# Performance work log

Hardware: AMD Instinct MI355X
Metric: run time of the kernel (lower is better)

Reference implementation:

```python
import jax, jax.numpy as jnp
import numpy as np

PAD_IDX = 0

def _gru_layer(xs, W_ih, W_hh, b_ih, b_hh):
    # xs: [B, S, D]; W_ih: [3H, D]; W_hh: [3H, H]
    B = xs.shape[0]
    H = W_hh.shape[1]
    # precompute input-side gate projections for all timesteps: [S, B, 3H]
    xg = jnp.einsum('bsd,gd->sbg', xs, W_ih) + b_ih

    def step(h, xg_t):
        hg = h @ W_hh.T + b_hh                      # [B, 3H]
        xr, xz, xn = jnp.split(xg_t, 3, axis=-1)
        hr, hz, hn = jnp.split(hg, 3, axis=-1)
        r = jax.nn.sigmoid(xr + hr)
        z = jax.nn.sigmoid(xz + hz)
        n = jnp.tanh(xn + r * hn)
        h_new = (1.0 - z) * n + z * h
        return h_new, h_new

    h0 = jnp.zeros((B, H), dtype=xs.dtype)
    _, ys = jax.lax.scan(step, h0, xg)              # ys: [S, B, H]
    return jnp.transpose(ys, (1, 0, 2))             # [B, S, H]

def setup_inputs() -> dict:
    key = jax.random.key(0)
    ks = jax.random.split(key, 12)
    V, E, H = 32000, 256, 512
    B, S = 64, 512
    s_e = 1.0 / np.sqrt(H)
    inp = {
        'x': jax.random.randint(ks[0], (B, S), 0, V, dtype=jnp.int32),
        'emb': jax.random.normal(ks[1], (V, E), dtype=jnp.float32),
        'W_ih0': jax.random.uniform(ks[2], (3 * H, E), jnp.float32, -s_e, s_e),
        'W_hh0': jax.random.uniform(ks[3], (3 * H, H), jnp.float32, -s_e, s_e),
        'b_ih0': jax.random.uniform(ks[4], (3 * H,), jnp.float32, -s_e, s_e),
        'b_hh0': jax.random.uniform(ks[5], (3 * H,), jnp.float32, -s_e, s_e),
        'W_ih1': jax.random.uniform(ks[6], (3 * H, H), jnp.float32, -s_e, s_e),
        'W_hh1': jax.random.uniform(ks[7], (3 * H, H), jnp.float32, -s_e, s_e),
        'b_ih1': jax.random.uniform(ks[8], (3 * H,), jnp.float32, -s_e, s_e),
        'b_hh1': jax.random.uniform(ks[9], (3 * H,), jnp.float32, -s_e, s_e),
        'W_fc': jax.random.uniform(ks[10], (1, H), jnp.float32, -s_e, s_e),
        'b_fc': jax.random.uniform(ks[11], (1,), jnp.float32, -s_e, s_e),
    }
    return inp

def reference(x, emb, W_ih0, W_hh0, b_ih0, b_hh0, W_ih1, W_hh1, b_ih1, b_hh1, W_fc, b_fc):
    # embedding with padding_idx: pad row is zero
    emb_z = emb.at[PAD_IDX].set(0.0)
    h = emb_z[x]                                    # [B, S, E]
    h = _gru_layer(h, W_ih0, W_hh0, b_ih0, b_hh0)   # [B, S, H]
    h = _gru_layer(h, W_ih1, W_hh1, b_ih1, b_hh1)   # [B, S, H]
    final = h[:, -1, :]                             # [B, H]
    return jax.nn.sigmoid(final @ W_fc.T + b_fc)    # [B, 1]
```

## Files before the change

### kernel.cpp

```cpp
#include <hip/hip_runtime.h>
#include <math.h>

typedef short  s8v __attribute__((ext_vector_type(8)));
typedef float  f4v __attribute__((ext_vector_type(4)));
typedef unsigned long long ull;

#define S_LEN 512
#define BATCH 64
#define HID   512
#define TPB   256

#define WI0H_OFF 0L
#define WI0L_OFF 786432L
#define WH0H_OFF 1572864L
#define WH0L_OFF 3145728L
#define WI1H_OFF 4718592L
#define WI1L_OFF 6291456L
#define WH1H_OFF 7864320L
#define WH1L_OFF 9437184L
#define XEB_OFF  11010048L
#define H0R_OFF  27787264L
#define H1R_OFF  94896128L
#define NEED_FAST 95420416L

#define BAR_BYTES   4096
#define HBUF_BYTES  (HID*BATCH*4)
#define A_OFF       BAR_BYTES
#define B_OFF       (A_OFF + 2*HBUF_BYTES)
#define XE_OFF      (B_OFF + 2*HBUF_BYTES)
#define XE_BYTES    ((size_t)S_LEN*64*BATCH*16)

__device__ __forceinline__ float fexp2(float x){ return __builtin_amdgcn_exp2f(x); }
__device__ __forceinline__ float frcp (float x){ return __builtin_amdgcn_rcpf(x); }
__device__ __forceinline__ float sigm (float x){ return frcp(1.f + fexp2(-1.44269504089f*x)); }
__device__ __forceinline__ float tanhx(float x){ return 1.f - 2.f*frcp(1.f + fexp2(2.88539008178f*x)); }
__device__ __forceinline__ float sigmoid_f(float v){ return 1.0f/(1.0f + expf(-v)); }

__device__ __forceinline__ unsigned short f2bf(float f){
  unsigned int u = __float_as_uint(f);
  u = u + 0x7FFFu + ((u >> 16) & 1u);
  return (unsigned short)(u >> 16);
}
__device__ __forceinline__ float bf2f(unsigned short s){
  return __uint_as_float(((unsigned int)s) << 16);
}

__global__ void wcvt_kernel(const float* __restrict__ Wih0, const float* __restrict__ Whh0,
                            const float* __restrict__ Wih1, const float* __restrict__ Whh1,
                            char* __restrict__ ws)
{
  int idx = blockIdx.x * TPB + threadIdx.x;
  const float* src; long hi_off, lo_off; int pos;
  if (idx < 393216)       { src = Wih0; pos = idx;           hi_off = WI0H_OFF; lo_off = WI0L_OFF; }
  else if (idx < 1179648) { src = Whh0; pos = idx - 393216;  hi_off = WH0H_OFF; lo_off = WH0L_OFF; }
  else if (idx < 1966080) { src = Wih1; pos = idx - 1179648; hi_off = WI1H_OFF; lo_off = WI1L_OFF; }
  else                    { src = Whh1; pos = idx - 1966080; hi_off = WH1H_OFF; lo_off = WH1L_OFF; }
  float w = src[pos];
  unsigned short h = f2bf(w);
  unsigned short l = f2bf(w - bf2f(h));
  ((unsigned short*)(ws + hi_off))[pos] = h;
  ((unsigned short*)(ws + lo_off))[pos] = l;
}

__global__ void gather_xe_bf_kernel(const int* __restrict__ x,
                                    const float* __restrict__ emb,
                                    char* __restrict__ ws)
{
  int idx = blockIdx.x * TPB + threadIdx.x;
  int k4 = idx & 63;
  int n  = idx >> 6;
  int t = n >> 6, b = n & 63;
  int tok = x[b * S_LEN + t];
  float4 v = make_float4(0.f,0.f,0.f,0.f);
  if (tok != 0) v = ((const float4*)emb)[(size_t)tok * 64 + k4];
  unsigned int lo = (unsigned int)f2bf(v.x) | ((unsigned int)f2bf(v.y) << 16);
  unsigned int hi = (unsigned int)f2bf(v.z) | ((unsigned int)f2bf(v.w) << 16);
  ((uint2*)(ws + XEB_OFF))[(long)n * 64 + k4] = make_uint2(lo, hi);
}

__device__ __forceinline__ void st_rec(ull* p, ull v){
  __hip_atomic_store(p, v, __ATOMIC_RELAXED, __HIP_MEMORY_SCOPE_AGENT);
}

template<int NKS>
__device__ __forceinline__ void load_ct(const ull* __restrict__ sl, int b,
                                        int quad, int k0s, unsigned want,
                                        s8v* __restrict__ bf)
{
  ull d[NKS][4];
  for (;;){
    #pragma unroll
    for (int ks = 0; ks < NKS; ++ks){
      const int e = k0s + ks*4 + quad;
      const ull* p = sl + (long)(4*e)*64 + b;
      #pragma unroll
      for (int i = 0; i < 4; ++i)
        d[ks][i] = __hip_atomic_load(p + (long)i*64, __ATOMIC_RELAXED, __HIP_MEMORY_SCOPE_AGENT);
    }
    bool ok = true;
    #pragma unroll
    for (int ks = 0; ks < NKS; ++ks)
      #pragma unroll
      for (int i = 0; i < 4; ++i)
        ok = ok && ((unsigned)(d[ks][i] >> 32) == want);
    if (__all(ok)) break;
    __builtin_amdgcn_s_sleep(1);
  }
  #pragma unroll
  for (int ks = 0; ks < NKS; ++ks){
    s8v v;
    #pragma unroll
    for (int i = 0; i < 4; ++i){
      unsigned lo = (unsigned)d[ks][i];
      v[2*i]   = (short)(lo & 0xFFFFu);
      v[2*i+1] = (short)(lo >> 16);
    }
    bf[ks] = v;
  }
}

template<int NKS, int ROLE>
__device__ __forceinline__ void scan_body(
    int isL1, int rowWG, int bh, int wave, int lane, int tid, int j0, int b0,
    const s8v* __restrict__ Whi, const s8v* __restrict__ Wlo, int AKs, int k0s,
    const s8v* __restrict__ xsrc,
    const ull* __restrict__ rsrc, int slotMask,
    const float* __restrict__ bih, const float* __restrict__ bhh,
    ull* __restrict__ rout, int outMask,
    f4v* __restrict__ part)
{
  const int quad = lane >> 4, col = lane & 15;

  s8v ahi[3][NKS], alo[3][NKS];
  #pragma unroll
  for (int rt = 0; rt < 3; ++rt){
    const int row = rt*512 + j0 + col;
    #pragma unroll
    for (int ks = 0; ks < NKS; ++ks){
      const int e = row*AKs + k0s + ks*4 + quad;
      ahi[rt][ks] = Whi[e];
      alo[rt][ks] = Wlo[e];
    }
  }

  float cr[4], cz[4], cnx[4], cnh[4], hp[4];
  #pragma unroll
  for (int r4 = 0; r4 < 4; ++r4){
    int j = j0 + wave*4 + r4;
    cr[r4]  = bih[j]      + bhh[j];
    cz[r4]  = bih[512+j]  + bhh[512+j];
    cnx[r4] = bih[1024+j];
    cnh[r4] = bhh[1024+j];
    hp[r4]  = 0.f;
  }

  for (int t = 0; t < S_LEN; ++t){
    f4v acc[3][2];
    #pragma unroll
    for (int rt = 0; rt < 3; ++rt){ acc[rt][0] = (f4v)0.f; acc[rt][1] = (f4v)0.f; }

    const bool active = (ROLE != 1) || (t > 0);
    if (active){
      const ull* sl = (ROLE == 1) ? rsrc + (long)((t-1) & slotMask)*16384
                                  : rsrc + (long)(t & slotMask)*16384;
      const unsigned want = (ROLE == 1) ? (unsigned)t : (unsigned)(t+1);
      #pragma unroll
      for (int ct = 0; ct < 2; ++ct){
        s8v bf[NKS];
        if (ROLE == 0){
          const int nG = b0 + ct*16 + col;
          const long base = ((long)t*64 + nG)*32 + k0s + quad;
          #pragma unroll
          for (int ks = 0; ks < NKS; ++ks) bf[ks] = xsrc[base + ks*4];
        } else {
          load_ct<NKS>(sl, b0 + ct*16 + col, quad, k0s, want, bf);
        }
        #pragma unroll
        for (int ks = 0; ks < NKS; ++ks)
          #pragma unroll
          for (int rt = 0; rt < 3; ++rt){
            acc[rt][ct] = __builtin_amdgcn_mfma_f32_16x16x32_bf16(ahi[rt][ks], bf[ks], acc[rt][ct], 0, 0, 0);
            acc[rt][ct] = __builtin_amdgcn_mfma_f32_16x16x32_bf16(alo[rt][ks], bf[ks], acc[rt][ct], 0, 0, 0);
          }
      }
    }

    #pragma unroll
    for (int rt = 0; rt < 3; ++rt)
      #pragma unroll
      for (int ct = 0; ct < 2; ++ct)
        part[(wave*6 + rt*2 + ct)*64 + lane] = acc[rt][ct];
    __syncthreads();

    if (lane < 32){
      const int b = lane;
      const int pl = wave*16 + (b & 15);
      const int ct = b >> 4;
      f4v sr = (f4v)0.f, sz = (f4v)0.f, snx = (f4v)0.f, snh = (f4v)0.f;
      #pragma unroll
      for (int w = 0; w < 4; ++w){
        const bool inpW = isL1 ? (w < 2) : (w >= 2);
        f4v g0 = part[(w*6 + 0*2 + ct)*64 + pl];
        f4v g1 = part[(w*6 + 1*2 + ct)*64 + pl];
        f4v g2 = part[(w*6 + 2*2 + ct)*64 + pl];
        sr += g0; sz += g1;
        if (inpW) snx += g2; else snh += g2;
      }
      unsigned short hb[4];
      #pragma unroll
      for (int r4 = 0; r4 < 4; ++r4){
        float r = sigm(sr[r4] + cr[r4]);
        float z = sigm(sz[r4] + cz[r4]);
        float n = tanhx(snx[r4] + cnx[r4] + r*(snh[r4] + cnh[r4]));
        float h = n + z*(hp[r4] - n);
        hp[r4] = h;
        hb[r4] = f2bf(h);
      }
      const int slotw = t & outMask;
      const ull tg = ((ull)(unsigned)(t + 1)) << 32;
      ull* ob = rout + (long)slotw*16384 + (long)(rowWG*8 + wave*2)*64 + (b0 + b);
      st_rec(ob,      ((ull)((unsigned)hb[0] | ((unsigned)hb[1] << 16))) | tg);
      st_rec(ob + 64, ((ull)((unsigned)hb[2] | ((unsigned)hb[3] << 16))) | tg);
    }
    __syncthreads();
  }
}

__global__ __launch_bounds__(TPB, 1) void gru_mfma_kernel(
    const float* __restrict__ bih0, const float* __restrict__ bhh0,
    const float* __restrict__ bih1, const float* __restrict__ bhh1,
    const float* __restrict__ Wfc,  const float* __restrict__ bfc,
    float* __restrict__ out, char* __restrict__ ws)
{
  __shared__ f4v part[4*6*64];

  const int tid  = threadIdx.x;
  const int wg   = blockIdx.x;
  const int lane = tid & 63;
  const int wave = tid >> 6;
  const int isL1 = (wg >= 64);
  const int lw   = wg & 63;
  const int rowWG = lw >> 1;
  const int bh    = lw & 1;
  const int j0 = rowWG * 16;
  const int b0 = bh * 32;

  const s8v* wi0h = (const s8v*)(ws + WI0H_OFF); const s8v* wi0l = (const s8v*)(ws + WI0L_OFF);
  const s8v* wh0h = (const s8v*)(ws + WH0H_OFF); const s8v* wh0l = (const s8v*)(ws + WH0L_OFF);
  const s8v* wi1h = (const s8v*)(ws + WI1H_OFF); const s8v* wi1l = (const s8v*)(ws + WI1L_OFF);
  const s8v* wh1h = (const s8v*)(ws + WH1H_OFF); const s8v* wh1l = (const s8v*)(ws + WH1L_OFF);
  const s8v* xeb = (const s8v*)(ws + XEB_OFF);
  const ull* h0r = (const ull*)(ws + H0R_OFF);
  const ull* h1r = (const ull*)(ws + H1R_OFF);
  ull* h0w = (ull*)(ws + H0R_OFF);
  ull* h1w = (ull*)(ws + H1R_OFF);

  if (!isL1){
    if (wave < 2)
      scan_body<8,1>(isL1, rowWG, bh, wave, lane, tid, j0, b0,
                     wh0h, wh0l, 64, wave*32, xeb, h0r, 0x3FFFFFFF,
                     bih0, bhh0, h0w, 0x3FFFFFFF, part);
    else
      scan_body<4,0>(isL1, rowWG, bh, wave, lane, tid, j0, b0,
                     wi0h, wi0l, 32, (wave-2)*16, xeb, h0r, 0x3FFFFFFF,
                     bih0, bhh0, h0w, 0x3FFFFFFF, part);
  } else {
    if (wave < 2)
      scan_body<8,2>(isL1, rowWG, bh, wave, lane, tid, j0, b0,
                     wi1h, wi1l, 64, wave*32, xeb, h0r, 0x3FFFFFFF,
                     bih1, bhh1, h1w, 3, part);
    else
      scan_body<8,1>(isL1, rowWG, bh, wave, lane, tid, j0, b0,
                     wh1h, wh1l, 64, (wave-2)*32, xeb, h1r, 3,
                     bih1, bhh1, h1w, 3, part);
  }

  if (wg == 64 && wave == 0){
    const ull* sl = h1r + 3L*16384;
    float acc = bfc[0];
    for (int c0 = 0; c0 < 256; c0 += 32){
      ull d[32];
      for (;;){
        #pragma unroll
        for (int i = 0; i < 32; ++i)
          d[i] = __hip_atomic_load(sl + (long)(c0+i)*64 + lane,
                                   __ATOMIC_RELAXED, __HIP_MEMORY_SCOPE_AGENT);
        bool ok = true;
        #pragma unroll
        for (int i = 0; i < 32; ++i) ok = ok && ((unsigned)(d[i] >> 32) == 512u);
        if (__all(ok)) break;
        __builtin_amdgcn_s_sleep(1);
      }
      #pragma unroll
      for (int i = 0; i < 32; ++i){
        unsigned lo = (unsigned)d[i];
        int u = (c0 + i) * 2;
        acc += bf2f((unsigned short)(lo & 0xFFFFu)) * Wfc[u]
             + bf2f((unsigned short)(lo >> 16))     * Wfc[u+1];
      }
    }
    out[lane] = sigm(acc);
  }
}

__global__ void gather_xe_kernel(const int* __restrict__ x,
                                 const float* __restrict__ emb,
                                 float4* __restrict__ xe4)
{
  int idx = blockIdx.x * TPB + threadIdx.x;
  int b  = idx & 63;
  int k4 = (idx >> 6) & 63;
  int t  = idx >> 12;
  int tok = x[b * S_LEN + t];
  float4 v = make_float4(0.f, 0.f, 0.f, 0.f);
  if (tok != 0) v = ((const float4*)emb)[(size_t)tok * 64 + k4];
  xe4[idx] = v;
}

__device__ __forceinline__ void accum_vec(const float4* __restrict__ xin,
                                          const float4* __restrict__ w0,
                                          const float4* __restrict__ w1,
                                          const float4* __restrict__ w2,
                                          int n4, int lane,
                                          float& ar, float& az, float& an)
{
  #pragma unroll 4
  for (int k = 0; k < n4; ++k){
    float4 xv = xin[k * 64 + lane];
    float4 wr = w0[k], wz = w1[k], wn = w2[k];
    ar = fmaf(xv.x, wr.x, ar); az = fmaf(xv.x, wz.x, az); an = fmaf(xv.x, wn.x, an);
    ar = fmaf(xv.y, wr.y, ar); az = fmaf(xv.y, wz.y, az); an = fmaf(xv.y, wn.y, an);
    ar = fmaf(xv.z, wr.z, ar); az = fmaf(xv.z, wz.z, az); an = fmaf(xv.z, wn.z, an);
    ar = fmaf(xv.w, wr.w, ar); az = fmaf(xv.w, wz.w, az); an = fmaf(xv.w, wn.w, an);
  }
}

__device__ __forceinline__ void accum_emb(const int* __restrict__ x,
                                          const float* __restrict__ emb, int t,
                                          const float4* __restrict__ w0,
                                          const float4* __restrict__ w1,
                                          const float4* __restrict__ w2,
                                          int lane, float& ar, float& az, float& an)
{
  int tok = x[lane * S_LEN + t];
  const float4* erow = (const float4*)emb + (size_t)tok * 64;
  float m = (tok != 0) ? 1.0f : 0.0f;
  #pragma unroll 4
  for (int k = 0; k < 64; ++k){
    float4 xv = erow[k];
    float xx = xv.x*m, xy = xv.y*m, xz = xv.z*m, xw = xv.w*m;
    float4 wr = w0[k], wz = w1[k], wn = w2[k];
    ar = fmaf(xx, wr.x, ar); az = fmaf(xx, wz.x, az); an = fmaf(xx, wn.x, an);
    ar = fmaf(xy, wr.y, ar); az = fmaf(xy, wz.y, az); an = fmaf(xy, wn.y, an);
    ar = fmaf(xz, wr.z, ar); az = fmaf(xz, wz.z, az); an = fmaf(xz, wn.z, an);
    ar = fmaf(xw, wr.w, ar); az = fmaf(xw, wz.w, az); an = fmaf(xw, wn.w, an);
  }
}

__device__ __forceinline__ void stage_weights(float4* wlds, int tid, int j0, int kin4,
                                              const float* Wih, const float* Whh)
{
  const int per = 3 * (kin4 + 128);
  for (int idx = tid; idx < 4 * per; idx += TPB){
    int w = idx / per, rem = idx - w * per;
    int g = rem / (kin4 + 128), k = rem - g * (kin4 + 128);
    int row = g * HID + j0 + w;
    float4 v;
    if (k < kin4) v = ((const float4*)Wih)[(size_t)row * kin4 + k];
    else          v = ((const float4*)Whh)[(size_t)row * 128 + (k - kin4)];
    wlds[(w * 3 + g) * 256 + k] = v;
  }
}

__device__ __forceinline__ void barrier_tick(int* bar, int wg, int tid, int phase)
{
  __syncthreads();
  if (tid == 0){
    __builtin_amdgcn_fence(__ATOMIC_RELEASE, "agent");
    int* leaf = bar + 32 + (wg >> 4) * 32;
    int old = __hip_atomic_fetch_add(leaf, 1, __ATOMIC_ACQ_REL, __HIP_MEMORY_SCOPE_AGENT);
    if (old == phase * 16 + 15){
      __hip_atomic_fetch_add(bar, 1, __ATOMIC_ACQ_REL, __HIP_MEMORY_SCOPE_AGENT);
    }
    const int target = (phase + 1) * 16;
    while (__hip_atomic_load(bar, __ATOMIC_ACQUIRE, __HIP_MEMORY_SCOPE_AGENT) < target){
      __builtin_amdgcn_s_sleep(2);
    }
    __builtin_amdgcn_fence(__ATOMIC_ACQUIRE, "agent");
  }
  __syncthreads();
}

__device__ __forceinline__ void finish_store(const float4* __restrict__ hprev,
                                             float ar, float az, float anx, float anh,
                                             int lane, int j, float4* __restrict__ hout)
{
  float r  = sigmoid_f(ar);
  float zz = sigmoid_f(az);
  float n  = tanhf(fmaf(r, anh, anx));
  int fi = ((j >> 2) * 64 + lane) * 4 + (j & 3);
  float hhp = ((const float*)hprev)[fi];
  ((float*)hout)[fi] = fmaf(zz, hhp - n, n);
}

__global__ __launch_bounds__(TPB) void gru_persist_kernel(
    const int*   __restrict__ x,    const float* __restrict__ emb,
    const float* __restrict__ Wih0, const float* __restrict__ Whh0,
    const float* __restrict__ bih0, const float* __restrict__ bhh0,
    const float* __restrict__ Wih1, const float* __restrict__ Whh1,
    const float* __restrict__ bih1, const float* __restrict__ bhh1,
    const float* __restrict__ Wfc,  const float* __restrict__ bfc,
    float* __restrict__ out, int* __restrict__ bar,
    float4* __restrict__ A0, float4* __restrict__ A1,
    float4* __restrict__ B0, float4* __restrict__ B1,
    const float4* __restrict__ xe4, int use_xe)
{
  __shared__ float4 wlds[3072];
  const int tid  = threadIdx.x;
  const int wg   = blockIdx.x;
  const int lane = tid & 63;
  const int wave = tid >> 6;
  const bool isL1 = (wg >= 128);
  const int j0   = (isL1 ? wg - 128 : wg) * 4;
  const int kin4 = isL1 ? 128 : 64;

  stage_weights(wlds, tid, j0, kin4, isL1 ? Wih1 : Wih0, isL1 ? Whh1 : Whh0);
  __syncthreads();

  const int j = j0 + wave;
  const float* bih = isL1 ? bih1 : bih0;
  const float* bhh = isL1 ? bhh1 : bhh0;
  const float br  = bih[j]        + bhh[j];
  const float bz  = bih[j + 512]  + bhh[j + 512];
  const float bnx = bih[j + 1024];
  const float bnh = bhh[j + 1024];

  const float4* w0 = &wlds[(wave * 3 + 0) * 256];
  const float4* w1 = &wlds[(wave * 3 + 1) * 256];
  const float4* w2 = &wlds[(wave * 3 + 2) * 256];

  float4* A[2] = {A0, A1};
  float4* B[2] = {B0, B1};

  for (int t = 0; t <= S_LEN; ++t){
    if (!isL1){
      if (t < S_LEN){
        const float4* hprev = A[(t + 1) & 1];
        float ar = br, az = bz, anx = bnx, anh = bnh;
        if (use_xe) accum_vec(xe4 + (size_t)t * 4096, w0, w1, w2, 64, lane, ar, az, anx);
        else        accum_emb(x, emb, t, w0, w1, w2, lane, ar, az, anx);
        accum_vec(hprev, w0 + 64, w1 + 64, w2 + 64, 128, lane, ar, az, anh);
        finish_store(hprev, ar, az, anx, anh, lane, j, A[t & 1]);
      }
    } else if (t >= 1){
      const int u = t - 1;
      const float4* xin   = A[u & 1];
      const float4* hprev = B[(u + 1) & 1];
      float ar = br, az = bz, anx = bnx, anh = bnh;
      accum_vec(xin,   w0,       w1,       w2,       128, lane, ar, az, anx);
      accum_vec(hprev, w0 + 128, w1 + 128, w2 + 128, 128, lane, ar, az, anh);
      finish_store(hprev, ar, az, anx, anh, lane, j, B[u & 1]);
    }
    barrier_tick(bar, wg, tid, t);
  }

  if (wg == 0 && wave == 0){
    float acc = bfc[0];
    const float4* h1 = B[1];
    const float4* wf = (const float4*)Wfc;
    #pragma unroll 4
    for (int k = 0; k < 128; ++k){
      float4 hv = h1[k * 64 + lane];
      float4 wv = wf[k];
      acc = fmaf(hv.x, wv.x, acc); acc = fmaf(hv.y, wv.y, acc);
      acc = fmaf(hv.z, wv.z, acc); acc = fmaf(hv.w, wv.w, acc);
    }
    out[lane] = sigmoid_f(acc);
  }
}

extern "C" void kernel_launch(void* const* d_in, const int* in_sizes, int n_in,
                              void* d_out, int out_size, void* d_ws, size_t ws_size,
                              hipStream_t stream)
{
  (void)in_sizes; (void)n_in; (void)out_size;
  const int*   x    = (const int*)  d_in[0];
  const float* emb  = (const float*)d_in[1];
  const float* Wih0 = (const float*)d_in[2];
  const float* Whh0 = (const float*)d_in[3];
  const float* bih0 = (const float*)d_in[4];
  const float* bhh0 = (const float*)d_in[5];
  const float* Wih1 = (const float*)d_in[6];
  const float* Whh1 = (const float*)d_in[7];
  const float* bih1 = (const float*)d_in[8];
  const float* bhh1 = (const float*)d_in[9];
  const float* Wfc  = (const float*)d_in[10];
  const float* bfc  = (const float*)d_in[11];
  float* out = (float*)d_out;
  char* ws = (char*)d_ws;

  if (ws_size >= (size_t)NEED_FAST){
    wcvt_kernel<<<2752512 / TPB, TPB, 0, stream>>>(Wih0, Whh0, Wih1, Whh1, ws);
    gather_xe_bf_kernel<<<2097152 / TPB, TPB, 0, stream>>>(x, emb, ws);
    gru_mfma_kernel<<<128, TPB, 0, stream>>>(bih0, bhh0, bih1, bhh1, Wfc, bfc, out, ws);
  } else {
    int*    bar = (int*)ws;
    float4* A0  = (float4*)(ws + A_OFF);
    float4* A1  = (float4*)(ws + A_OFF + HBUF_BYTES);
    float4* B0  = (float4*)(ws + B_OFF);
    float4* B1  = (float4*)(ws + B_OFF + HBUF_BYTES);
    float4* xe4 = (float4*)(ws + XE_OFF);
    const int use_xe = (ws_size >= (size_t)XE_OFF + XE_BYTES) ? 1 : 0;
    hipMemsetAsync(ws, 0, XE_OFF, stream);
    if (use_xe){
      gather_xe_kernel<<<(S_LEN * 64 * BATCH) / TPB, TPB, 0, stream>>>(x, emb, xe4);
    }
    gru_persist_kernel<<<256, TPB, 0, stream>>>(
        x, emb, Wih0, Whh0, bih0, bhh0, Wih1, Whh1, bih1, bhh1, Wfc, bfc,
        out, bar, A0, A1, B0, B1, xe4, use_xe);
  }
}
```

Before: 2.036 ms.

## Transpose recurrent state layout, vectorize tagged loads/stores, double-buffer LDS partials

```diff
diff --git a/kernel.cpp b/kernel.cpp
--- a/kernel.cpp
+++ b/kernel.cpp
@@ -3,6 +3,7 @@
 
 typedef short  s8v __attribute__((ext_vector_type(8)));
 typedef float  f4v __attribute__((ext_vector_type(4)));
+typedef unsigned int u4v __attribute__((ext_vector_type(4)));
 typedef unsigned long long ull;
 
 #define S_LEN 512
@@ -78,47 +79,6 @@
   ((uint2*)(ws + XEB_OFF))[(long)n * 64 + k4] = make_uint2(lo, hi);
 }
 
-__device__ __forceinline__ void st_rec(ull* p, ull v){
-  __hip_atomic_store(p, v, __ATOMIC_RELAXED, __HIP_MEMORY_SCOPE_AGENT);
-}
-
-template<int NKS>
-__device__ __forceinline__ void load_ct(const ull* __restrict__ sl, int b,
-                                        int quad, int k0s, unsigned want,
-                                        s8v* __restrict__ bf)
-{
-  ull d[NKS][4];
-  for (;;){
-    #pragma unroll
-    for (int ks = 0; ks < NKS; ++ks){
-      const int e = k0s + ks*4 + quad;
-      const ull* p = sl + (long)(4*e)*64 + b;
-      #pragma unroll
-      for (int i = 0; i < 4; ++i)
-        d[ks][i] = __hip_atomic_load(p + (long)i*64, __ATOMIC_RELAXED, __HIP_MEMORY_SCOPE_AGENT);
-    }
-    bool ok = true;
-    #pragma unroll
-    for (int ks = 0; ks < NKS; ++ks)
-      #pragma unroll
-      for (int i = 0; i < 4; ++i)
-        ok = ok && ((unsigned)(d[ks][i] >> 32) == want);
-    if (__all(ok)) break;
-    __builtin_amdgcn_s_sleep(1);
-  }
-  #pragma unroll
-  for (int ks = 0; ks < NKS; ++ks){
-    s8v v;
-    #pragma unroll
-    for (int i = 0; i < 4; ++i){
-      unsigned lo = (unsigned)d[ks][i];
-      v[2*i]   = (short)(lo & 0xFFFFu);
-      v[2*i+1] = (short)(lo >> 16);
-    }
-    bf[ks] = v;
-  }
-}
-
 template<int NKS, int ROLE>
 __device__ __forceinline__ void scan_body(
     int isL1, int rowWG, int bh, int wave, int lane, int tid, int j0, int b0,
@@ -159,21 +119,69 @@
     #pragma unroll
     for (int rt = 0; rt < 3; ++rt){ acc[rt][0] = (f4v)0.f; acc[rt][1] = (f4v)0.f; }
 
-    const bool active = (ROLE != 1) || (t > 0);
-    if (active){
-      const ull* sl = (ROLE == 1) ? rsrc + (long)((t-1) & slotMask)*16384
-                                  : rsrc + (long)(t & slotMask)*16384;
-      const unsigned want = (ROLE == 1) ? (unsigned)t : (unsigned)(t+1);
+    if (ROLE == 0){
       #pragma unroll
       for (int ct = 0; ct < 2; ++ct){
+        const int nG = b0 + ct*16 + col;
+        const long base = ((long)t*64 + nG)*32 + k0s + quad;
         s8v bf[NKS];
-        if (ROLE == 0){
-          const int nG = b0 + ct*16 + col;
-          const long base = ((long)t*64 + nG)*32 + k0s + quad;
+        #pragma unroll
+        for (int ks = 0; ks < NKS; ++ks) bf[ks] = xsrc[base + ks*4];
+        #pragma unroll
+        for (int ks = 0; ks < NKS; ++ks)
           #pragma unroll
-          for (int ks = 0; ks < NKS; ++ks) bf[ks] = xsrc[base + ks*4];
-        } else {
-          load_ct<NKS>(sl, b0 + ct*16 + col, quad, k0s, want, bf);
+          for (int rt = 0; rt < 3; ++rt){
+            acc[rt][ct] = __builtin_amdgcn_mfma_f32_16x16x32_bf16(ahi[rt][ks], bf[ks], acc[rt][ct], 0, 0, 0);
+            acc[rt][ct] = __builtin_amdgcn_mfma_f32_16x16x32_bf16(alo[rt][ks], bf[ks], acc[rt][ct], 0, 0, 0);
+          }
+      }
+    } else if ((ROLE != 1) || (t > 0)){
+      const int slot = (ROLE == 1) ? ((t-1) & slotMask) : (t & slotMask);
+      const unsigned want = (ROLE == 1) ? (unsigned)t : (unsigned)(t+1);
+      const ull* sl = rsrc + (long)slot*16384;
+
+      {
+        const ull* pp = sl + (long)(b0 + (lane & 31))*256 + (4*k0s + 2*lane);
+        for (;;){
+          u4v pv;
+          asm volatile("global_load_dwordx4 %0, %1, off sc0 sc1\n\t"
+                       "s_waitcnt vmcnt(0)"
+                       : "=&v"(pv) : "v"(pp) : "memory");
+          if (__all((pv.y == want) && (pv.w == want))) break;
+          __builtin_amdgcn_s_sleep(2);
+        }
+      }
+
+      #pragma unroll
+      for (int ct = 0; ct < 2; ++ct){
+        const int b = b0 + ct*16 + col;
+        const ull* bb = sl + (long)b*256 + (4*k0s + 4*quad);
+        s8v bf[NKS];
+        for (;;){
+          u4v q0[NKS], q1[NKS];
+          #pragma unroll
+          for (int ks = 0; ks < NKS; ++ks){
+            const ull* a = bb + 16*ks;
+            asm volatile("global_load_dwordx4 %0, %1, off sc0 sc1"
+                         : "=&v"(q0[ks]) : "v"(a) : "memory");
+            asm volatile("global_load_dwordx4 %0, %1, off sc0 sc1"
+                         : "=&v"(q1[ks]) : "v"(a + 2) : "memory");
+          }
+          asm volatile("s_waitcnt vmcnt(0)" ::: "memory");
+          bool ok = true;
+          #pragma unroll
+          for (int ks = 0; ks < NKS; ++ks)
+            ok = ok && (q0[ks].y == want) && (q0[ks].w == want)
+                    && (q1[ks].y == want) && (q1[ks].w == want);
+          if (__all(ok)){
+            #pragma unroll
+            for (int ks = 0; ks < NKS; ++ks){
+              u4v tv; tv.x = q0[ks].x; tv.y = q0[ks].z; tv.z = q1[ks].x; tv.w = q1[ks].z;
+              bf[ks] = *(s8v*)&tv;
+            }
+            break;
+          }
+          __builtin_amdgcn_s_sleep(2);
         }
         #pragma unroll
         for (int ks = 0; ks < NKS; ++ks)
@@ -185,11 +193,12 @@
       }
     }
 
+    const int pb = t & 1;
     #pragma unroll
     for (int rt = 0; rt < 3; ++rt)
       #pragma unroll
       for (int ct = 0; ct < 2; ++ct)
-        part[(wave*6 + rt*2 + ct)*64 + lane] = acc[rt][ct];
+        part[((pb*4 + wave)*6 + rt*2 + ct)*64 + lane] = acc[rt][ct];
     __syncthreads();
 
     if (lane < 32){
@@ -200,9 +209,9 @@
       #pragma unroll
       for (int w = 0; w < 4; ++w){
         const bool inpW = isL1 ? (w < 2) : (w >= 2);
-        f4v g0 = part[(w*6 + 0*2 + ct)*64 + pl];
-        f4v g1 = part[(w*6 + 1*2 + ct)*64 + pl];
-        f4v g2 = part[(w*6 + 2*2 + ct)*64 + pl];
+        f4v g0 = part[((pb*4 + w)*6 + 0*2 + ct)*64 + pl];
+        f4v g1 = part[((pb*4 + w)*6 + 1*2 + ct)*64 + pl];
+        f4v g2 = part[((pb*4 + w)*6 + 2*2 + ct)*64 + pl];
         sr += g0; sz += g1;
         if (inpW) snx += g2; else snh += g2;
       }
@@ -217,12 +226,13 @@
         hb[r4] = f2bf(h);
       }
       const int slotw = t & outMask;
-      const ull tg = ((ull)(unsigned)(t + 1)) << 32;
-      ull* ob = rout + (long)slotw*16384 + (long)(rowWG*8 + wave*2)*64 + (b0 + b);
-      st_rec(ob,      ((ull)((unsigned)hb[0] | ((unsigned)hb[1] << 16))) | tg);
-      st_rec(ob + 64, ((ull)((unsigned)hb[2] | ((unsigned)hb[3] << 16))) | tg);
-    }
-    __syncthreads();
+      const unsigned tg = (unsigned)(t + 1);
+      u4v sv;
+      sv.x = (unsigned)hb[0] | ((unsigned)hb[1] << 16); sv.y = tg;
+      sv.z = (unsigned)hb[2] | ((unsigned)hb[3] << 16); sv.w = tg;
+      ull* ob = rout + (long)slotw*16384 + (long)(b0 + b)*256 + (rowWG*8 + wave*2);
+      asm volatile("global_store_dwordx4 %0, %1, off sc0 sc1" :: "v"(ob), "v"(sv) : "memory");
+    }
   }
 }
 
@@ -232,7 +242,7 @@
     const float* __restrict__ Wfc,  const float* __restrict__ bfc,
     float* __restrict__ out, char* __restrict__ ws)
 {
-  __shared__ f4v part[4*6*64];
+  __shared__ f4v part[3072];
 
   const int tid  = threadIdx.x;
   const int wg   = blockIdx.x;
@@ -276,15 +286,14 @@
   }
 
   if (wg == 64 && wave == 0){
-    const ull* sl = h1r + 3L*16384;
+    const ull* bb = h1r + 3L*16384 + (long)lane*256;
     float acc = bfc[0];
     for (int c0 = 0; c0 < 256; c0 += 32){
       ull d[32];
       for (;;){
         #pragma unroll
         for (int i = 0; i < 32; ++i)
-          d[i] = __hip_atomic_load(sl + (long)(c0+i)*64 + lane,
-                                   __ATOMIC_RELAXED, __HIP_MEMORY_SCOPE_AGENT);
+          d[i] = __hip_atomic_load(bb + c0 + i, __ATOMIC_RELAXED, __HIP_MEMORY_SCOPE_AGENT);
         bool ok = true;
         #pragma unroll
         for (int i = 0; i < 32; ++i) ok = ok && ((unsigned)(d[i] >> 32) == 512u);
```

Measured after the change: 3.238 ms. 1.59x slower.

## Add per-group progress flags and double-buffer partials to drop second block barrier

Applied to the files above, without the earlier changes.

```diff
diff --git a/kernel.cpp b/kernel.cpp
--- a/kernel.cpp
+++ b/kernel.cpp
@@ -21,7 +21,8 @@
 #define XEB_OFF  11010048L
 #define H0R_OFF  27787264L
 #define H1R_OFF  94896128L
-#define NEED_FAST 95420416L
+#define FLG_OFF  95420416L
+#define NEED_FAST 95422464L
 
 #define BAR_BYTES   4096
 #define HBUF_BYTES  (HID*BATCH*4)
@@ -81,31 +82,36 @@
 __device__ __forceinline__ void st_rec(ull* p, ull v){
   __hip_atomic_store(p, v, __ATOMIC_RELAXED, __HIP_MEMORY_SCOPE_AGENT);
 }
+__device__ __forceinline__ void hint_wait(const unsigned* fl, int lane, unsigned target){
+  const unsigned* p = fl + (lane & 31);
+  for (;;){
+    unsigned v = __hip_atomic_load(p, __ATOMIC_RELAXED, __HIP_MEMORY_SCOPE_AGENT);
+    if (__all(v >= target)) break;
+    __builtin_amdgcn_s_sleep(1);
+  }
+}
 
 template<int NKS>
-__device__ __forceinline__ void load_ct(const ull* __restrict__ sl, int b,
-                                        int quad, int k0s, unsigned want,
-                                        s8v* __restrict__ bf)
+__device__ __forceinline__ bool try_load(const ull* __restrict__ sl, int b,
+                                         int quad, int k0s, unsigned want,
+                                         s8v* __restrict__ bf)
 {
   ull d[NKS][4];
-  for (;;){
+  #pragma unroll
+  for (int ks = 0; ks < NKS; ++ks){
+    const int e = k0s + ks*4 + quad;
+    const ull* p = sl + (long)(4*e)*64 + b;
     #pragma unroll
-    for (int ks = 0; ks < NKS; ++ks){
-      const int e = k0s + ks*4 + quad;
-      const ull* p = sl + (long)(4*e)*64 + b;
-      #pragma unroll
-      for (int i = 0; i < 4; ++i)
-        d[ks][i] = __hip_atomic_load(p + (long)i*64, __ATOMIC_RELAXED, __HIP_MEMORY_SCOPE_AGENT);
-    }
-    bool ok = true;
+    for (int i = 0; i < 4; ++i)
+      d[ks][i] = __hip_atomic_load(p + (long)i*64, __ATOMIC_RELAXED, __HIP_MEMORY_SCOPE_AGENT);
+  }
+  bool ok = true;
+  #pragma unroll
+  for (int ks = 0; ks < NKS; ++ks)
     #pragma unroll
-    for (int ks = 0; ks < NKS; ++ks)
-      #pragma unroll
-      for (int i = 0; i < 4; ++i)
-        ok = ok && ((unsigned)(d[ks][i] >> 32) == want);
-    if (__all(ok)) break;
-    __builtin_amdgcn_s_sleep(1);
-  }
+    for (int i = 0; i < 4; ++i)
+      ok = ok && ((unsigned)(d[ks][i] >> 32) == want);
+  if (!__all(ok)) return false;
   #pragma unroll
   for (int ks = 0; ks < NKS; ++ks){
     s8v v;
@@ -117,17 +123,18 @@
     }
     bf[ks] = v;
   }
+  return true;
 }
 
 template<int NKS, int ROLE>
 __device__ __forceinline__ void scan_body(
-    int isL1, int rowWG, int bh, int wave, int lane, int tid, int j0, int b0,
+    int isL1, int rowWG, int bh, int wave, int lane, int j0, int b0,
     const s8v* __restrict__ Whi, const s8v* __restrict__ Wlo, int AKs, int k0s,
     const s8v* __restrict__ xsrc,
     const ull* __restrict__ rsrc, int slotMask,
     const float* __restrict__ bih, const float* __restrict__ bhh,
     ull* __restrict__ rout, int outMask,
-    f4v* __restrict__ part)
+    char* __restrict__ ws, f4v* __restrict__ part, unsigned* __restrict__ cnt)
 {
   const int quad = lane >> 4, col = lane & 15;
 
@@ -154,26 +161,50 @@
     hp[r4]  = 0.f;
   }
 
+  const int pollLayer = (ROLE == 2) ? 0 : isL1;
+  const unsigned* flg = (const unsigned*)(ws + FLG_OFF)
+                        + ((pollLayer*2 + bh)*4 + (rowWG & 3))*32;
+  unsigned* fpub = (unsigned*)(ws + FLG_OFF) + ((isL1*2 + bh)*4)*32 + rowWG;
+
   for (int t = 0; t < S_LEN; ++t){
     f4v acc[3][2];
     #pragma unroll
     for (int rt = 0; rt < 3; ++rt){ acc[rt][0] = (f4v)0.f; acc[rt][1] = (f4v)0.f; }
 
-    const bool active = (ROLE != 1) || (t > 0);
-    if (active){
-      const ull* sl = (ROLE == 1) ? rsrc + (long)((t-1) & slotMask)*16384
-                                  : rsrc + (long)(t & slotMask)*16384;
-      const unsigned want = (ROLE == 1) ? (unsigned)t : (unsigned)(t+1);
+    if (ROLE == 0){
       #pragma unroll
       for (int ct = 0; ct < 2; ++ct){
+        const int nG = b0 + ct*16 + col;
+        const long base = ((long)t*64 + nG)*32 + k0s + quad;
         s8v bf[NKS];
-        if (ROLE == 0){
-          const int nG = b0 + ct*16 + col;
-          const long base = ((long)t*64 + nG)*32 + k0s + quad;
+        #pragma unroll
+        for (int ks = 0; ks < NKS; ++ks) bf[ks] = xsrc[base + ks*4];
+        #pragma unroll
+        for (int ks = 0; ks < NKS; ++ks)
           #pragma unroll
-          for (int ks = 0; ks < NKS; ++ks) bf[ks] = xsrc[base + ks*4];
+          for (int rt = 0; rt < 3; ++rt){
+            acc[rt][ct] = __builtin_amdgcn_mfma_f32_16x16x32_bf16(ahi[rt][ks], bf[ks], acc[rt][ct], 0, 0, 0);
+            acc[rt][ct] = __builtin_amdgcn_mfma_f32_16x16x32_bf16(alo[rt][ks], bf[ks], acc[rt][ct], 0, 0, 0);
+          }
+      }
+    } else if ((ROLE != 1) || (t > 0)){
+      const int slot = (ROLE == 1) ? ((t-1) & slotMask) : (t & slotMask);
+      const unsigned want = (ROLE == 1) ? (unsigned)t : (unsigned)(t+1);
+      const ull* sl = rsrc + (long)slot*16384;
+      #pragma unroll
+      for (int ct = 0; ct < 2; ++ct){
+        const int b = b0 + ct*16 + col;
+        s8v bf[NKS];
+        if (ROLE == 2){
+          if (!try_load<NKS>(sl, b, quad, k0s, want, bf)){
+            hint_wait(flg, lane, want);
+            while (!try_load<NKS>(sl, b, quad, k0s, want, bf))
+              __builtin_amdgcn_s_sleep(1);
+          }
         } else {
-          load_ct<NKS>(sl, b0 + ct*16 + col, quad, k0s, want, bf);
+          if (ct == 0) hint_wait(flg, lane, want);
+          while (!try_load<NKS>(sl, b, quad, k0s, want, bf))
+            __builtin_amdgcn_s_sleep(1);
         }
         #pragma unroll
         for (int ks = 0; ks < NKS; ++ks)
@@ -185,11 +216,12 @@
       }
     }
 
+    const int pb = t & 1;
     #pragma unroll
     for (int rt = 0; rt < 3; ++rt)
       #pragma unroll
       for (int ct = 0; ct < 2; ++ct)
-        part[(wave*6 + rt*2 + ct)*64 + lane] = acc[rt][ct];
+        part[((pb*4 + wave)*6 + rt*2 + ct)*64 + lane] = acc[rt][ct];
     __syncthreads();
 
     if (lane < 32){
@@ -200,9 +232,9 @@
       #pragma unroll
       for (int w = 0; w < 4; ++w){
         const bool inpW = isL1 ? (w < 2) : (w >= 2);
-        f4v g0 = part[(w*6 + 0*2 + ct)*64 + pl];
-        f4v g1 = part[(w*6 + 1*2 + ct)*64 + pl];
-        f4v g2 = part[(w*6 + 2*2 + ct)*64 + pl];
+        f4v g0 = part[((pb*4 + w)*6 + 0*2 + ct)*64 + pl];
+        f4v g1 = part[((pb*4 + w)*6 + 1*2 + ct)*64 + pl];
+        f4v g2 = part[((pb*4 + w)*6 + 2*2 + ct)*64 + pl];
         sr += g0; sz += g1;
         if (inpW) snx += g2; else snh += g2;
       }
@@ -222,7 +254,15 @@
       st_rec(ob,      ((ull)((unsigned)hb[0] | ((unsigned)hb[1] << 16))) | tg);
       st_rec(ob + 64, ((ull)((unsigned)hb[2] | ((unsigned)hb[3] << 16))) | tg);
     }
-    __syncthreads();
+    if (lane == 0){
+      unsigned old = atomicAdd(cnt, 1u);
+      if (old == 4u*(unsigned)t + 3u){
+        #pragma unroll
+        for (int rp = 0; rp < 4; ++rp)
+          __hip_atomic_store(fpub + rp*32, (unsigned)(t + 1),
+                             __ATOMIC_RELAXED, __HIP_MEMORY_SCOPE_AGENT);
+      }
+    }
   }
 }
 
@@ -232,7 +272,8 @@
     const float* __restrict__ Wfc,  const float* __restrict__ bfc,
     float* __restrict__ out, char* __restrict__ ws)
 {
-  __shared__ f4v part[4*6*64];
+  __shared__ f4v part[3072];
+  __shared__ unsigned cnt;
 
   const int tid  = threadIdx.x;
   const int wg   = blockIdx.x;
@@ -245,6 +286,9 @@
   const int j0 = rowWG * 16;
   const int b0 = bh * 32;
 
+  if (tid == 0) cnt = 0;
+  __syncthreads();
+
   const s8v* wi0h = (const s8v*)(ws + WI0H_OFF); const s8v* wi0l = (const s8v*)(ws + WI0L_OFF);
   const s8v* wh0h = (const s8v*)(ws + WH0H_OFF); const s8v* wh0l = (const s8v*)(ws + WH0L_OFF);
   const s8v* wi1h = (const s8v*)(ws + WI1H_OFF); const s8v* wi1l = (const s8v*)(ws + WI1L_OFF);
@@ -257,22 +301,22 @@
 
   if (!isL1){
     if (wave < 2)
-      scan_body<8,1>(isL1, rowWG, bh, wave, lane, tid, j0, b0,
+      scan_body<8,1>(isL1, rowWG, bh, wave, lane, j0, b0,
                      wh0h, wh0l, 64, wave*32, xeb, h0r, 0x3FFFFFFF,
-                     bih0, bhh0, h0w, 0x3FFFFFFF, part);
+                     bih0, bhh0, h0w, 0x3FFFFFFF, ws, part, &cnt);
     else
-      scan_body<4,0>(isL1, rowWG, bh, wave, lane, tid, j0, b0,
+      scan_body<4,0>(isL1, rowWG, bh, wave, lane, j0, b0,
                      wi0h, wi0l, 32, (wave-2)*16, xeb, h0r, 0x3FFFFFFF,
-                     bih0, bhh0, h0w, 0x3FFFFFFF, part);
+                     bih0, bhh0, h0w, 0x3FFFFFFF, ws, part, &cnt);
   } else {
     if (wave < 2)
-      scan_body<8,2>(isL1, rowWG, bh, wave, lane, tid, j0, b0,
+      scan_body<8,2>(isL1, rowWG, bh, wave, lane, j0, b0,
                      wi1h, wi1l, 64, wave*32, xeb, h0r, 0x3FFFFFFF,
-                     bih1, bhh1, h1w, 3, part);
+                     bih1, bhh1, h1w, 3, ws, part, &cnt);
     else
-      scan_body<8,1>(isL1, rowWG, bh, wave, lane, tid, j0, b0,
+      scan_body<8,1>(isL1, rowWG, bh, wave, lane, j0, b0,
                      wh1h, wh1l, 64, (wave-2)*32, xeb, h1r, 3,
-                     bih1, bhh1, h1w, 3, part);
+                     bih1, bhh1, h1w, 3, ws, part, &cnt);
   }
 
   if (wg == 64 && wave == 0){
@@ -500,6 +544,7 @@
   char* ws = (char*)d_ws;
 
   if (ws_size >= (size_t)NEED_FAST){
+    hipMemsetAsync(ws + FLG_OFF, 0, 2048, stream);
     wcvt_kernel<<<2752512 / TPB, TPB, 0, stream>>>(Wih0, Whh0, Wih1, Whh1, ws);
     gather_xe_bf_kernel<<<2097152 / TPB, TPB, 0, stream>>>(x, emb, ws);
     gru_mfma_kernel<<<128, TPB, 0, stream>>>(bih0, bhh0, bih1, bhh1, Wfc, bfc, out, ws);
```

New measurement: 2.681 ms. +31.7%, slower.

## Split recurrent K-dim across all four waves and double-buffer gate partials

Applied to the files above, without the earlier changes.

```diff
diff --git a/kernel.cpp b/kernel.cpp
--- a/kernel.cpp
+++ b/kernel.cpp
@@ -82,30 +82,37 @@
   __hip_atomic_store(p, v, __ATOMIC_RELAXED, __HIP_MEMORY_SCOPE_AGENT);
 }
 
+__device__ __forceinline__ void poll_slice(const ull* __restrict__ sl, int recBase,
+                                           int b0, int lane, unsigned want){
+  const ull* p = sl + (long)(recBase + lane)*64 + (b0 + (lane & 31));
+  for (;;){
+    ull v = __hip_atomic_load(p, __ATOMIC_RELAXED, __HIP_MEMORY_SCOPE_AGENT);
+    if (__all((unsigned)(v >> 32) == want)) break;
+    __builtin_amdgcn_s_sleep(1);
+  }
+}
+
 template<int NKS>
-__device__ __forceinline__ void load_ct(const ull* __restrict__ sl, int b,
-                                        int quad, int k0s, unsigned want,
-                                        s8v* __restrict__ bf)
+__device__ __forceinline__ bool try_load(const ull* __restrict__ sl, int b,
+                                         int quad, int k0s, unsigned want,
+                                         s8v* __restrict__ bf)
 {
   ull d[NKS][4];
-  for (;;){
-    #pragma unroll
-    for (int ks = 0; ks < NKS; ++ks){
-      const int e = k0s + ks*4 + quad;
-      const ull* p = sl + (long)(4*e)*64 + b;
-      #pragma unroll
-      for (int i = 0; i < 4; ++i)
-        d[ks][i] = __hip_atomic_load(p + (long)i*64, __ATOMIC_RELAXED, __HIP_MEMORY_SCOPE_AGENT);
-    }
-    bool ok = true;
-    #pragma unroll
-    for (int ks = 0; ks < NKS; ++ks)
-      #pragma unroll
-      for (int i = 0; i < 4; ++i)
-        ok = ok && ((unsigned)(d[ks][i] >> 32) == want);
-    if (__all(ok)) break;
-    __builtin_amdgcn_s_sleep(1);
-  }
+  #pragma unroll
+  for (int ks = 0; ks < NKS; ++ks){
+    const int e = k0s + ks*4 + quad;
+    const ull* p = sl + (long)(4*e)*64 + b;
+    #pragma unroll
+    for (int i = 0; i < 4; ++i)
+      d[ks][i] = __hip_atomic_load(p + (long)i*64, __ATOMIC_RELAXED, __HIP_MEMORY_SCOPE_AGENT);
+  }
+  bool ok = true;
+  #pragma unroll
+  for (int ks = 0; ks < NKS; ++ks)
+    #pragma unroll
+    for (int i = 0; i < 4; ++i)
+      ok = ok && ((unsigned)(d[ks][i] >> 32) == want);
+  if (!__all(ok)) return false;
   #pragma unroll
   for (int ks = 0; ks < NKS; ++ks){
     s8v v;
@@ -117,29 +124,42 @@
     }
     bf[ks] = v;
   }
-}
-
-template<int NKS, int ROLE>
+  return true;
+}
+
+#define MF(A,B,C) __builtin_amdgcn_mfma_f32_16x16x32_bf16((A),(B),(C),0,0,0)
+
+template<int NKSI, int LAYER>
 __device__ __forceinline__ void scan_body(
-    int isL1, int rowWG, int bh, int wave, int lane, int tid, int j0, int b0,
-    const s8v* __restrict__ Whi, const s8v* __restrict__ Wlo, int AKs, int k0s,
-    const s8v* __restrict__ xsrc,
-    const ull* __restrict__ rsrc, int slotMask,
+    int rowWG, int bh, int wave, int lane, int j0, int b0,
+    const s8v* __restrict__ Wih_hi, const s8v* __restrict__ Wih_lo, int AKi,
+    const s8v* __restrict__ Whh_hi, const s8v* __restrict__ Whh_lo,
+    const s8v* __restrict__ xeb,
+    const ull* __restrict__ insrc,
+    const ull* __restrict__ hsrc, int hMask,
     const float* __restrict__ bih, const float* __restrict__ bhh,
     ull* __restrict__ rout, int outMask,
     f4v* __restrict__ part)
 {
   const int quad = lane >> 4, col = lane & 15;
-
-  s8v ahi[3][NKS], alo[3][NKS];
+  const int k0i = wave * (NKSI*4);
+  const int k0h = wave * 16;
+
+  s8v aih[3][NKSI], ail[3][NKSI], ahh[3][4], ahl[3][4];
   #pragma unroll
   for (int rt = 0; rt < 3; ++rt){
     const int row = rt*512 + j0 + col;
     #pragma unroll
-    for (int ks = 0; ks < NKS; ++ks){
-      const int e = row*AKs + k0s + ks*4 + quad;
-      ahi[rt][ks] = Whi[e];
-      alo[rt][ks] = Wlo[e];
+    for (int ks = 0; ks < NKSI; ++ks){
+      const int e = row*AKi + k0i + ks*4 + quad;
+      aih[rt][ks] = Wih_hi[e];
+      ail[rt][ks] = Wih_lo[e];
+    }
+    #pragma unroll
+    for (int ks = 0; ks < 4; ++ks){
+      const int e = row*64 + k0h + ks*4 + quad;
+      ahh[rt][ks] = Whh_hi[e];
+      ahl[rt][ks] = Whh_lo[e];
     }
   }
 
@@ -155,41 +175,80 @@
   }
 
   for (int t = 0; t < S_LEN; ++t){
-    f4v acc[3][2];
-    #pragma unroll
-    for (int rt = 0; rt < 3; ++rt){ acc[rt][0] = (f4v)0.f; acc[rt][1] = (f4v)0.f; }
-
-    const bool active = (ROLE != 1) || (t > 0);
-    if (active){
-      const ull* sl = (ROLE == 1) ? rsrc + (long)((t-1) & slotMask)*16384
-                                  : rsrc + (long)(t & slotMask)*16384;
-      const unsigned want = (ROLE == 1) ? (unsigned)t : (unsigned)(t+1);
+    f4v acc[4][2];
+    #pragma unroll
+    for (int c = 0; c < 4; ++c){ acc[c][0] = (f4v)0.f; acc[c][1] = (f4v)0.f; }
+
+    if (LAYER == 0){
       #pragma unroll
       for (int ct = 0; ct < 2; ++ct){
-        s8v bf[NKS];
-        if (ROLE == 0){
-          const int nG = b0 + ct*16 + col;
-          const long base = ((long)t*64 + nG)*32 + k0s + quad;
-          #pragma unroll
-          for (int ks = 0; ks < NKS; ++ks) bf[ks] = xsrc[base + ks*4];
-        } else {
-          load_ct<NKS>(sl, b0 + ct*16 + col, quad, k0s, want, bf);
+        const int nG = b0 + ct*16 + col;
+        const long base = ((long)t*64 + nG)*32 + k0i + quad;
+        s8v bf[NKSI];
+        #pragma unroll
+        for (int ks = 0; ks < NKSI; ++ks) bf[ks] = xeb[base + ks*4];
+        #pragma unroll
+        for (int ks = 0; ks < NKSI; ++ks){
+          acc[0][ct] = MF(aih[0][ks], bf[ks], acc[0][ct]);
+          acc[0][ct] = MF(ail[0][ks], bf[ks], acc[0][ct]);
+          acc[1][ct] = MF(aih[1][ks], bf[ks], acc[1][ct]);
+          acc[1][ct] = MF(ail[1][ks], bf[ks], acc[1][ct]);
+          acc[2][ct] = MF(aih[2][ks], bf[ks], acc[2][ct]);
+          acc[2][ct] = MF(ail[2][ks], bf[ks], acc[2][ct]);
+        }
+      }
+    } else {
+      const ull* sl = insrc + (long)t*16384;
+      const unsigned want = (unsigned)(t + 1);
+      #pragma unroll
+      for (int ct = 0; ct < 2; ++ct){
+        const int b = b0 + ct*16 + col;
+        s8v bf[NKSI];
+        if (!try_load<NKSI>(sl, b, quad, k0i, want, bf)){
+          poll_slice(sl, 4*k0i, b0, lane, want);
+          while (!try_load<NKSI>(sl, b, quad, k0i, want, bf))
+            __builtin_amdgcn_s_sleep(1);
         }
         #pragma unroll
-        for (int ks = 0; ks < NKS; ++ks)
-          #pragma unroll
-          for (int rt = 0; rt < 3; ++rt){
-            acc[rt][ct] = __builtin_amdgcn_mfma_f32_16x16x32_bf16(ahi[rt][ks], bf[ks], acc[rt][ct], 0, 0, 0);
-            acc[rt][ct] = __builtin_amdgcn_mfma_f32_16x16x32_bf16(alo[rt][ks], bf[ks], acc[rt][ct], 0, 0, 0);
-          }
-      }
-    }
-
-    #pragma unroll
-    for (int rt = 0; rt < 3; ++rt)
+        for (int ks = 0; ks < NKSI; ++ks){
+          acc[0][ct] = MF(aih[0][ks], bf[ks], acc[0][ct]);
+          acc[0][ct] = MF(ail[0][ks], bf[ks], acc[0][ct]);
+          acc[1][ct] = MF(aih[1][ks], bf[ks], acc[1][ct]);
+          acc[1][ct] = MF(ail[1][ks], bf[ks], acc[1][ct]);
+          acc[2][ct] = MF(aih[2][ks], bf[ks], acc[2][ct]);
+          acc[2][ct] = MF(ail[2][ks], bf[ks], acc[2][ct]);
+        }
+      }
+    }
+
+    if (t > 0){
+      const ull* sl = hsrc + (long)((t-1) & hMask)*16384;
+      const unsigned want = (unsigned)t;
+      poll_slice(sl, 4*k0h, b0, lane, want);
+      #pragma unroll
+      for (int ct = 0; ct < 2; ++ct){
+        const int b = b0 + ct*16 + col;
+        s8v bf[4];
+        while (!try_load<4>(sl, b, quad, k0h, want, bf))
+          __builtin_amdgcn_s_sleep(1);
+        #pragma unroll
+        for (int ks = 0; ks < 4; ++ks){
+          acc[0][ct] = MF(ahh[0][ks], bf[ks], acc[0][ct]);
+          acc[0][ct] = MF(ahl[0][ks], bf[ks], acc[0][ct]);
+          acc[1][ct] = MF(ahh[1][ks], bf[ks], acc[1][ct]);
+          acc[1][ct] = MF(ahl[1][ks], bf[ks], acc[1][ct]);
+          acc[3][ct] = MF(ahh[2][ks], bf[ks], acc[3][ct]);
+          acc[3][ct] = MF(ahl[2][ks], bf[ks], acc[3][ct]);
+        }
+      }
+    }
+
+    const int pb = t & 1;
+    #pragma unroll
+    for (int c = 0; c < 4; ++c)
       #pragma unroll
       for (int ct = 0; ct < 2; ++ct)
-        part[(wave*6 + rt*2 + ct)*64 + lane] = acc[rt][ct];
+        part[((pb*4 + wave)*8 + c*2 + ct)*64 + lane] = acc[c][ct];
     __syncthreads();
 
     if (lane < 32){
@@ -199,12 +258,10 @@
       f4v sr = (f4v)0.f, sz = (f4v)0.f, snx = (f4v)0.f, snh = (f4v)0.f;
       #pragma unroll
       for (int w = 0; w < 4; ++w){
-        const bool inpW = isL1 ? (w < 2) : (w >= 2);
-        f4v g0 = part[(w*6 + 0*2 + ct)*64 + pl];
-        f4v g1 = part[(w*6 + 1*2 + ct)*64 + pl];
-        f4v g2 = part[(w*6 + 2*2 + ct)*64 + pl];
-        sr += g0; sz += g1;
-        if (inpW) snx += g2; else snh += g2;
+        sr  += part[((pb*4 + w)*8 + 0*2 + ct)*64 + pl];
+        sz  += part[((pb*4 + w)*8 + 1*2 + ct)*64 + pl];
+        snx += part[((pb*4 + w)*8 + 2*2 + ct)*64 + pl];
+        snh += part[((pb*4 + w)*8 + 3*2 + ct)*64 + pl];
       }
       unsigned short hb[4];
       #pragma unroll
@@ -222,7 +279,6 @@
       st_rec(ob,      ((ull)((unsigned)hb[0] | ((unsigned)hb[1] << 16))) | tg);
       st_rec(ob + 64, ((ull)((unsigned)hb[2] | ((unsigned)hb[3] << 16))) | tg);
     }
-    __syncthreads();
   }
 }
 
@@ -232,7 +288,7 @@
     const float* __restrict__ Wfc,  const float* __restrict__ bfc,
     float* __restrict__ out, char* __restrict__ ws)
 {
-  __shared__ f4v part[4*6*64];
+  __shared__ f4v part[4096];
 
   const int tid  = threadIdx.x;
   const int wg   = blockIdx.x;
@@ -256,23 +312,15 @@
   ull* h1w = (ull*)(ws + H1R_OFF);
 
   if (!isL1){
-    if (wave < 2)
-      scan_body<8,1>(isL1, rowWG, bh, wave, lane, tid, j0, b0,
-                     wh0h, wh0l, 64, wave*32, xeb, h0r, 0x3FFFFFFF,
-                     bih0, bhh0, h0w, 0x3FFFFFFF, part);
-    else
-      scan_body<4,0>(isL1, rowWG, bh, wave, lane, tid, j0, b0,
-                     wi0h, wi0l, 32, (wave-2)*16, xeb, h0r, 0x3FFFFFFF,
-                     bih0, bhh0, h0w, 0x3FFFFFFF, part);
+    scan_body<2,0>(rowWG, bh, wave, lane, j0, b0,
+                   wi0h, wi0l, 32, wh0h, wh0l, xeb,
+                   (const ull*)0, h0r, 0x3FFFFFFF,
+                   bih0, bhh0, h0w, 0x3FFFFFFF, part);
   } else {
-    if (wave < 2)
-      scan_body<8,2>(isL1, rowWG, bh, wave, lane, tid, j0, b0,
-                     wi1h, wi1l, 64, wave*32, xeb, h0r, 0x3FFFFFFF,
-                     bih1, bhh1, h1w, 3, part);
-    else
-      scan_body<8,1>(isL1, rowWG, bh, wave, lane, tid, j0, b0,
-                     wh1h, wh1l, 64, (wave-2)*32, xeb, h1r, 3,
-                     bih1, bhh1, h1w, 3, part);
+    scan_body<4,1>(rowWG, bh, wave, lane, j0, b0,
+                   wi1h, wi1l, 64, wh1h, wh1l, xeb,
+                   h0r, h1r, 3,
+                   bih1, bhh1, h1w, 3, part);
   }
 
   if (wg == 64 && wave == 0){
```

Result: slower. 2.550 ms (+25.3%).
